# Optimization experiments

Measured on AMD Instinct MI355X. Metric: run time of the kernel, lower is better.

## Reference

```python
import jax, jax.numpy as jnp
import numpy as np

B, SQ, SK, H, A = 4, 512, 512, 256, 128

def setup_inputs() -> dict:
    key = jax.random.key(0)
    ks = jax.random.split(key, 8)
    s = 1.0 / np.sqrt(H)
    sa = 1.0 / np.sqrt(A)
    return {
        "Q": jax.random.normal(ks[0], (B, SQ, H), dtype=jnp.float32),
        "K": jax.random.normal(ks[1], (B, SK, H), dtype=jnp.float32),
        "V": jax.random.normal(ks[2], (B, SK, H), dtype=jnp.float32),
        "W_q": jax.random.uniform(ks[3], (H, A), jnp.float32, -s, s),
        "W_k": jax.random.uniform(ks[4], (H, A), jnp.float32, -s, s),
        "v": jax.random.uniform(ks[5], (A,), jnp.float32, -sa, sa),
        "W_o": jax.random.uniform(ks[6], (H, H), jnp.float32, -s, s),
        "b_o": jax.random.uniform(ks[7], (H,), jnp.float32, -s, s),
    }

def reference(Q, K, V, W_q, W_k, v, W_o, b_o):
    # Q: (B, Sq, H), K/V: (B, Sk, H)
    Qt = Q @ W_q                      # (B, Sq, A)
    Kt = K @ W_k                      # (B, Sk, A)
    additive = jnp.tanh(Qt[:, :, None, :] + Kt[:, None, :, :])  # (B, Sq, Sk, A)
    scores = jnp.einsum('bqka,a->bqk', additive, v)             # (B, Sq, Sk)
    weights = jax.nn.softmax(scores, axis=-1)                   # (B, Sq, Sk)
    out = jnp.einsum('bqk,bkh->bqh', weights, V)                 # (B, Sq, H)
    out = out @ W_o + b_o
    return (out, weights)
```

## Files before the change

### kernel.cpp

```cpp
#include <hip/hip_runtime.h>
#include <math.h>

#define BB 4
#define SQL 512
#define SKL 512
#define HH 256
#define AA 128

#define PRESCALE 2.8853900817779268f

__device__ inline void fma4(float4& a, float s, const float4& b) {
    a.x = fmaf(s, b.x, a.x); a.y = fmaf(s, b.y, a.y);
    a.z = fmaf(s, b.z, a.z); a.w = fmaf(s, b.w, a.w);
}

__device__ inline unsigned short f_to_bf16(float f) {
    unsigned u = __float_as_uint(f);
    return (unsigned short)((u + 0x7fffu + ((u >> 16) & 1u)) >> 16);
}
__device__ inline float4 bf16x4_to_f4(uint2 u) {
    float4 r;
    r.x = __uint_as_float(u.x << 16);
    r.y = __uint_as_float(u.x & 0xffff0000u);
    r.z = __uint_as_float(u.y << 16);
    r.w = __uint_as_float(u.y & 0xffff0000u);
    return r;
}

__global__ __launch_bounds__(256) void prep_kernel(
    const float* __restrict__ Q, const float* __restrict__ K,
    const float* __restrict__ V,
    const float* __restrict__ Wq, const float* __restrict__ Wk,
    const float* __restrict__ Wo,
    float* __restrict__ Qt, float* __restrict__ Kt,
    unsigned short* __restrict__ VW)
{
    __shared__ float rows[16 * 260];
    __shared__ float wbuf[2][32 * 64];
    int tid = threadIdx.x;
    int bid = blockIdx.x;

    const float* X; const float* W;
    int ldW, col0, r0, kind;
    if (bid < 256)      { X=Q; W=Wq; ldW=AA; kind=0; r0=(bid>>1)*16;       col0=(bid&1)*64; }
    else if (bid < 512) { X=K; W=Wk; ldW=AA; kind=1; r0=((bid-256)>>1)*16; col0=((bid-256)&1)*64; }
    else { int b2=bid-512; X=V; W=Wo; ldW=HH; kind=2; r0=(b2>>2)*16;       col0=(b2&3)*64; }

    {
        const float4* Xv = (const float4*)(X + (size_t)r0 * HH);
        #pragma unroll
        for (int it = 0; it < 4; ++it) {
            int l = tid + it * 256;
            int rr = l >> 6, cc = (l & 63) << 2;
            *(float4*)&rows[rr * 260 + cc] = Xv[l];
        }
    }

    float4 wpf0, wpf1;
    {
        int l0 = tid, l1 = tid + 256;
        wpf0 = *(const float4*)(W + (size_t)(l0 >> 4) * ldW + col0 + ((l0 & 15) << 2));
        wpf1 = *(const float4*)(W + (size_t)(l1 >> 4) * ldW + col0 + ((l1 & 15) << 2));
    }

    int r  = tid >> 4;
    int c4 = tid & 15;
    float4 acc = {0.f, 0.f, 0.f, 0.f};

    for (int c = 0; c < 8; ++c) {
        {
            float4* wb = (float4*)&wbuf[c & 1][0];
            wb[tid]       = wpf0;
            wb[tid + 256] = wpf1;
            if (c < 7) {
                const float* Wb = W + (size_t)((c + 1) * 32) * ldW + col0;
                int l0 = tid, l1 = tid + 256;
                wpf0 = *(const float4*)(Wb + (size_t)(l0 >> 4) * ldW + ((l0 & 15) << 2));
                wpf1 = *(const float4*)(Wb + (size_t)(l1 >> 4) * ldW + ((l1 & 15) << 2));
            }
        }
        __syncthreads();
        const float* rrow = &rows[r * 260 + c * 32];
        const float* wb2  = &wbuf[c & 1][c4 << 2];
        #pragma unroll
        for (int h = 0; h < 32; ++h) {
            float rv  = rrow[h];
            float4 w4 = *(const float4*)(wb2 + h * 64);
            fma4(acc, rv, w4);
        }
    }

    if (kind < 2) {
        float* Y = (kind == 0) ? Qt : Kt;
        acc.x *= PRESCALE; acc.y *= PRESCALE; acc.z *= PRESCALE; acc.w *= PRESCALE;
        *(float4*)(Y + (size_t)(r0 + r) * AA + col0 + (c4 << 2)) = acc;
    } else {
        ushort4 s = { f_to_bf16(acc.x), f_to_bf16(acc.y),
                      f_to_bf16(acc.z), f_to_bf16(acc.w) };
        *(ushort4*)(VW + (size_t)(r0 + r) * HH + col0 + (c4 << 2)) = s;
    }
}

__global__ __launch_bounds__(256) void score_part(
    const float* __restrict__ Qt, const float* __restrict__ Kt,
    const float* __restrict__ v,  float* __restrict__ scores)
{
    __shared__ float sc[2][256];

    int tid = threadIdx.x;
    int bid = blockIdx.x;
    int b    = bid >> 9;
    int rem  = bid & 511;
    int q0   = rem & ~1;
    int half = rem & 1;
    int ag = tid & 15;
    int kl = tid >> 4;

    float q0r[8], dr[8], v2[8];
    {
        const float4* vp  = (const float4*)(v + ag * 8);
        const float4* qp0 = (const float4*)(Qt + (size_t)(b * SQL + q0)     * AA + ag * 8);
        const float4* qp1 = (const float4*)(Qt + (size_t)(b * SQL + q0 + 1) * AA + ag * 8);
        #pragma unroll
        for (int j4 = 0; j4 < 2; ++j4) {
            float4 vv4 = vp[j4];
            float4 a0  = qp0[j4];
            float4 a1  = qp1[j4];
            *(float4*)&q0r[j4 * 4] = a0;
            dr[j4*4+0] = __builtin_amdgcn_exp2f(a1.x - a0.x);
            dr[j4*4+1] = __builtin_amdgcn_exp2f(a1.y - a0.y);
            dr[j4*4+2] = __builtin_amdgcn_exp2f(a1.z - a0.z);
            dr[j4*4+3] = __builtin_amdgcn_exp2f(a1.w - a0.w);
            v2[j4*4+0] = 2.0f * vv4.x;
            v2[j4*4+1] = 2.0f * vv4.y;
            v2[j4*4+2] = 2.0f * vv4.z;
            v2[j4*4+3] = 2.0f * vv4.w;
        }
    }

    float S_all;
    {
        float ls = 0.f;
        #pragma unroll
        for (int j = 0; j < 8; ++j) ls += v2[j];
        ls += __shfl_xor(ls, 1);
        ls += __shfl_xor(ls, 2);
        ls += __shfl_xor(ls, 4);
        ls += __shfl_xor(ls, 8);
        S_all = 0.5f * ls;
    }

    const float4* kp = (const float4*)(Kt + (size_t)(b * SKL + half * 256 + kl) * AA + ag * 8);
    float4 n0 = kp[0], n1 = kp[1];
    for (int c = 0; c < 16; ++c) {
        float kt[8];
        *(float4*)&kt[0] = n0;
        *(float4*)&kt[4] = n1;
        if (c < 15) {
            const float4* np = kp + (size_t)(c + 1) * 16 * (AA / 4);
            n0 = np[0]; n1 = np[1];
        }
        float p0 = 0.f, p1 = 0.f;
        #pragma unroll
        for (int j = 0; j < 8; ++j) {
            float x0 = q0r[j] + kt[j];
            float e0 = __builtin_amdgcn_exp2f(x0);
            float e1 = e0 * dr[j];
            float r0 = __builtin_amdgcn_rcpf(e0 + 1.0f);
            float r1 = __builtin_amdgcn_rcpf(e1 + 1.0f);
            p0 = fmaf(v2[j], r0, p0);
            p1 = fmaf(v2[j], r1, p1);
        }
        p0 += __shfl_xor(p0, 1); p1 += __shfl_xor(p1, 1);
        p0 += __shfl_xor(p0, 2); p1 += __shfl_xor(p1, 2);
        p0 += __shfl_xor(p0, 4); p1 += __shfl_xor(p1, 4);
        p0 += __shfl_xor(p0, 8); p1 += __shfl_xor(p1, 8);
        if (ag == 0) {
            sc[0][c * 16 + kl] = S_all - p0;
            sc[1][c * 16 + kl] = S_all - p1;
        }
    }
    __syncthreads();

    if (tid < 128) {
        int q = tid >> 6, i = tid & 63;
        float4 val = *(float4*)&sc[q][i << 2];
        *(float4*)(scores + (size_t)(b * SQL + q0 + q) * SKL + half * 256 + (i << 2)) = val;
    }
}

__global__ __launch_bounds__(256) void softepi_kernel(
    const unsigned short* __restrict__ VW, const float* __restrict__ bo,
    float* __restrict__ weights, float* __restrict__ out)
{
    __shared__ float sw[2][SKL];
    __shared__ float pout[4][2][HH];
    __shared__ float pm[2][2], ps[2][2];

    int tid = threadIdx.x;
    int b  = blockIdx.x >> 8;
    int q0 = (blockIdx.x & 255) << 1;
    int wave = tid >> 6, lane = tid & 63;
    int qi = wave & 1, half = wave >> 1;

    {
        float* wrow = weights + (size_t)(b * SQL + q0 + qi) * SKL + half * 256;
        float4 sv = *(float4*)(wrow + (lane << 2));
        float m = fmaxf(fmaxf(sv.x, sv.y), fmaxf(sv.z, sv.w));
        #pragma unroll
        for (int off = 32; off; off >>= 1) m = fmaxf(m, __shfl_xor(m, off));
        if (lane == 0) pm[qi][half] = m;
        __syncthreads();
        float M = fmaxf(pm[qi][0], pm[qi][1]);
        float4 e;
        e.x = __builtin_amdgcn_exp2f((sv.x - M) * 1.44269504f);
        e.y = __builtin_amdgcn_exp2f((sv.y - M) * 1.44269504f);
        e.z = __builtin_amdgcn_exp2f((sv.z - M) * 1.44269504f);
        e.w = __builtin_amdgcn_exp2f((sv.w - M) * 1.44269504f);
        float s = (e.x + e.y) + (e.z + e.w);
        #pragma unroll
        for (int off = 32; off; off >>= 1) s += __shfl_xor(s, off);
        if (lane == 0) ps[qi][half] = s;
        __syncthreads();
        float rinv = 1.0f / (ps[qi][0] + ps[qi][1]);
        float4 w4 = { e.x * rinv, e.y * rinv, e.z * rinv, e.w * rinv };
        *(float4*)&sw[qi][half * 256 + (lane << 2)] = w4;
        *(float4*)(wrow + (lane << 2)) = w4;
    }
    __syncthreads();

    {
        const uint2* VWb = (const uint2*)(VW + (size_t)b * SKL * HH);
        float4 a0 = {0,0,0,0}, a1 = {0,0,0,0};
        int kbase = wave * 128;
        #pragma unroll 4
        for (int k = 0; k < 128; ++k) {
            int kk = kbase + k;
            uint2 u = VWb[(size_t)kk * (HH / 4) + lane];
            float4 vw4 = bf16x4_to_f4(u);
            float w0 = sw[0][kk];
            float w1 = sw[1][kk];
            fma4(a0, w0, vw4);
            fma4(a1, w1, vw4);
        }
        *(float4*)&pout[wave][0][lane << 2] = a0;
        *(float4*)&pout[wave][1][lane << 2] = a1;
    }
    __syncthreads();
    {
        int h = tid;
        float bias = bo[h];
        #pragma unroll
        for (int q2 = 0; q2 < 2; ++q2) {
            float s = bias + pout[0][q2][h] + pout[1][q2][h]
                           + pout[2][q2][h] + pout[3][q2][h];
            out[(size_t)(b * SQL + q0 + q2) * HH + h] = s;
        }
    }
}

extern "C" void kernel_launch(void* const* d_in, const int* in_sizes, int n_in,
                              void* d_out, int out_size, void* d_ws, size_t ws_size,
                              hipStream_t stream)
{
    const float* Q  = (const float*)d_in[0];
    const float* K  = (const float*)d_in[1];
    const float* V  = (const float*)d_in[2];
    const float* Wq = (const float*)d_in[3];
    const float* Wk = (const float*)d_in[4];
    const float* v  = (const float*)d_in[5];
    const float* Wo = (const float*)d_in[6];
    const float* bo = (const float*)d_in[7];

    float* out     = (float*)d_out;
    float* weights = out + (size_t)BB * SQL * HH;

    float* Qt = (float*)d_ws;
    float* Kt = Qt + (size_t)BB * SQL * AA;
    unsigned short* VW = (unsigned short*)(Kt + (size_t)BB * SKL * AA);

    prep_kernel <<<1024, 256, 0, stream>>>(Q, K, V, Wq, Wk, Wo, Qt, Kt, VW);
    score_part  <<<2048, 256, 0, stream>>>(Qt, Kt, v, weights);
    softepi_kernel<<<1024, 256, 0, stream>>>(VW, bo, weights, out);
}
```

Measured before the change: 130.8 us.

## Register-tile prep GEMM, widen score lanes, vectorize weight reads in epilogue

The projection kernel now keeps W tiles in registers with double-buffered global loads. It stores X transposed in LDS so each thread computes two output rows by 4 columns, and it halves the grid. The score kernel gives each thread 16 attention dimensions instead of 8, which drops one shuffle stage per reduction but raises register use. The softmax-epilogue loop reads weights as float4 and issues four VW loads per iteration for more memory-level parallelism.

```diff
diff --git a/kernel.cpp b/kernel.cpp
--- a/kernel.cpp
+++ b/kernel.cpp
@@ -35,69 +35,92 @@
     float* __restrict__ Qt, float* __restrict__ Kt,
     unsigned short* __restrict__ VW)
 {
-    __shared__ float rows[16 * 260];
-    __shared__ float wbuf[2][32 * 64];
+    __shared__ float rowsT[256 * 18 + 2];
     int tid = threadIdx.x;
     int bid = blockIdx.x;
 
     const float* X; const float* W;
     int ldW, col0, r0, kind;
-    if (bid < 256)      { X=Q; W=Wq; ldW=AA; kind=0; r0=(bid>>1)*16;       col0=(bid&1)*64; }
-    else if (bid < 512) { X=K; W=Wk; ldW=AA; kind=1; r0=((bid-256)>>1)*16; col0=((bid-256)&1)*64; }
-    else { int b2=bid-512; X=V; W=Wo; ldW=HH; kind=2; r0=(b2>>2)*16;       col0=(b2&3)*64; }
+    if (bid < 128)      { X=Q; W=Wq; ldW=AA; kind=0; r0=bid*16;        col0=0; }
+    else if (bid < 256) { X=K; W=Wk; ldW=AA; kind=1; r0=(bid-128)*16;  col0=0; }
+    else { int b2=bid-256; X=V; W=Wo; ldW=HH; kind=2; r0=(b2>>1)*16; col0=(b2&1)*128; }
+
+    int mg = tid >> 5;
+    int n4 = tid & 31;
+    int rpair = mg << 1;
+    const float* Wg = W + col0 + (n4 << 2);
+
+    float4 wA[8], wB[8];
+    #pragma unroll
+    for (int j = 0; j < 8; ++j)
+        wA[j] = *(const float4*)(Wg + (size_t)j * ldW);
 
     {
         const float4* Xv = (const float4*)(X + (size_t)r0 * HH);
         #pragma unroll
         for (int it = 0; it < 4; ++it) {
             int l = tid + it * 256;
-            int rr = l >> 6, cc = (l & 63) << 2;
-            *(float4*)&rows[rr * 260 + cc] = Xv[l];
-        }
-    }
-
-    float4 wpf0, wpf1;
-    {
-        int l0 = tid, l1 = tid + 256;
-        wpf0 = *(const float4*)(W + (size_t)(l0 >> 4) * ldW + col0 + ((l0 & 15) << 2));
-        wpf1 = *(const float4*)(W + (size_t)(l1 >> 4) * ldW + col0 + ((l1 & 15) << 2));
-    }
-
-    int r  = tid >> 4;
-    int c4 = tid & 15;
-    float4 acc = {0.f, 0.f, 0.f, 0.f};
-
-    for (int c = 0; c < 8; ++c) {
+            int r = l >> 6, h4 = (l & 63) << 2;
+            float4 x = Xv[l];
+            rowsT[(h4 + 0) * 18 + r] = x.x;
+            rowsT[(h4 + 1) * 18 + r] = x.y;
+            rowsT[(h4 + 2) * 18 + r] = x.z;
+            rowsT[(h4 + 3) * 18 + r] = x.w;
+        }
+    }
+    __syncthreads();
+
+    float2 aA[8], aB[8];
+    #pragma unroll
+    for (int j = 0; j < 8; ++j)
+        aA[j] = *(const float2*)&rowsT[j * 18 + rpair];
+
+    float4 accA = {0,0,0,0}, accB = {0,0,0,0};
+
+    for (int g = 0; g < 32; g += 2) {
         {
-            float4* wb = (float4*)&wbuf[c & 1][0];
-            wb[tid]       = wpf0;
-            wb[tid + 256] = wpf1;
-            if (c < 7) {
-                const float* Wb = W + (size_t)((c + 1) * 32) * ldW + col0;
-                int l0 = tid, l1 = tid + 256;
-                wpf0 = *(const float4*)(Wb + (size_t)(l0 >> 4) * ldW + ((l0 & 15) << 2));
-                wpf1 = *(const float4*)(Wb + (size_t)(l1 >> 4) * ldW + ((l1 & 15) << 2));
+            const float* Wb = Wg + (size_t)((g + 1) * 8) * ldW;
+            int hb = (g + 1) * 8;
+            #pragma unroll
+            for (int j = 0; j < 8; ++j) {
+                wB[j] = *(const float4*)(Wb + (size_t)j * ldW);
+                aB[j] = *(const float2*)&rowsT[(hb + j) * 18 + rpair];
             }
         }
-        __syncthreads();
-        const float* rrow = &rows[r * 260 + c * 32];
-        const float* wb2  = &wbuf[c & 1][c4 << 2];
-        #pragma unroll
-        for (int h = 0; h < 32; ++h) {
-            float rv  = rrow[h];
-            float4 w4 = *(const float4*)(wb2 + h * 64);
-            fma4(acc, rv, w4);
+        #pragma unroll
+        for (int j = 0; j < 8; ++j) {
+            fma4(accA, aA[j].x, wA[j]);
+            fma4(accB, aA[j].y, wA[j]);
+        }
+        if (g + 2 < 32) {
+            const float* Wb = Wg + (size_t)((g + 2) * 8) * ldW;
+            int hb = (g + 2) * 8;
+            #pragma unroll
+            for (int j = 0; j < 8; ++j) {
+                wA[j] = *(const float4*)(Wb + (size_t)j * ldW);
+                aA[j] = *(const float2*)&rowsT[(hb + j) * 18 + rpair];
+            }
+        }
+        #pragma unroll
+        for (int j = 0; j < 8; ++j) {
+            fma4(accA, aB[j].x, wB[j]);
+            fma4(accB, aB[j].y, wB[j]);
         }
     }
 
     if (kind < 2) {
         float* Y = (kind == 0) ? Qt : Kt;
-        acc.x *= PRESCALE; acc.y *= PRESCALE; acc.z *= PRESCALE; acc.w *= PRESCALE;
-        *(float4*)(Y + (size_t)(r0 + r) * AA + col0 + (c4 << 2)) = acc;
+        accA.x *= PRESCALE; accA.y *= PRESCALE; accA.z *= PRESCALE; accA.w *= PRESCALE;
+        accB.x *= PRESCALE; accB.y *= PRESCALE; accB.z *= PRESCALE; accB.w *= PRESCALE;
+        *(float4*)(Y + (size_t)(r0 + rpair)     * AA + (n4 << 2)) = accA;
+        *(float4*)(Y + (size_t)(r0 + rpair + 1) * AA + (n4 << 2)) = accB;
     } else {
-        ushort4 s = { f_to_bf16(acc.x), f_to_bf16(acc.y),
-                      f_to_bf16(acc.z), f_to_bf16(acc.w) };
-        *(ushort4*)(VW + (size_t)(r0 + r) * HH + col0 + (c4 << 2)) = s;
+        ushort4 sa = { f_to_bf16(accA.x), f_to_bf16(accA.y),
+                       f_to_bf16(accA.z), f_to_bf16(accA.w) };
+        ushort4 sb = { f_to_bf16(accB.x), f_to_bf16(accB.y),
+                       f_to_bf16(accB.z), f_to_bf16(accB.w) };
+        *(ushort4*)(VW + (size_t)(r0 + rpair)     * HH + col0 + (n4 << 2)) = sa;
+        *(ushort4*)(VW + (size_t)(r0 + rpair + 1) * HH + col0 + (n4 << 2)) = sb;
     }
 }
 
@@ -113,16 +136,16 @@
     int rem  = bid & 511;
     int q0   = rem & ~1;
     int half = rem & 1;
-    int ag = tid & 15;
-    int kl = tid >> 4;
-
-    float q0r[8], dr[8], v2[8];
-    {
-        const float4* vp  = (const float4*)(v + ag * 8);
-        const float4* qp0 = (const float4*)(Qt + (size_t)(b * SQL + q0)     * AA + ag * 8);
-        const float4* qp1 = (const float4*)(Qt + (size_t)(b * SQL + q0 + 1) * AA + ag * 8);
-        #pragma unroll
-        for (int j4 = 0; j4 < 2; ++j4) {
+    int ag = tid & 7;
+    int kl = tid >> 3;
+
+    float q0r[16], dr[16], v2[16];
+    {
+        const float4* vp  = (const float4*)(v + ag * 16);
+        const float4* qp0 = (const float4*)(Qt + (size_t)(b * SQL + q0)     * AA + ag * 16);
+        const float4* qp1 = (const float4*)(Qt + (size_t)(b * SQL + q0 + 1) * AA + ag * 16);
+        #pragma unroll
+        for (int j4 = 0; j4 < 4; ++j4) {
             float4 vv4 = vp[j4];
             float4 a0  = qp0[j4];
             float4 a1  = qp1[j4];
@@ -142,27 +165,29 @@
     {
         float ls = 0.f;
         #pragma unroll
-        for (int j = 0; j < 8; ++j) ls += v2[j];
+        for (int j = 0; j < 16; ++j) ls += v2[j];
         ls += __shfl_xor(ls, 1);
         ls += __shfl_xor(ls, 2);
         ls += __shfl_xor(ls, 4);
-        ls += __shfl_xor(ls, 8);
         S_all = 0.5f * ls;
     }
 
-    const float4* kp = (const float4*)(Kt + (size_t)(b * SKL + half * 256 + kl) * AA + ag * 8);
-    float4 n0 = kp[0], n1 = kp[1];
-    for (int c = 0; c < 16; ++c) {
-        float kt[8];
-        *(float4*)&kt[0] = n0;
-        *(float4*)&kt[4] = n1;
-        if (c < 15) {
-            const float4* np = kp + (size_t)(c + 1) * 16 * (AA / 4);
-            n0 = np[0]; n1 = np[1];
-        }
+    const float4* kp = (const float4*)(Kt + (size_t)(b * SKL + half * 256 + kl) * AA + ag * 16);
+    float4 n0 = kp[0], n1 = kp[1], n2 = kp[2], n3 = kp[3];
+    for (int c = 0; c < 8; ++c) {
+        float kt[16];
+        *(float4*)&kt[0]  = n0;
+        *(float4*)&kt[4]  = n1;
+        *(float4*)&kt[8]  = n2;
+        *(float4*)&kt[12] = n3;
+        if (c < 7) {
+            const float4* np = kp + (size_t)(c + 1) * 32 * (AA / 4);
+            n0 = np[0]; n1 = np[1]; n2 = np[2]; n3 = np[3];
+        }
+
         float p0 = 0.f, p1 = 0.f;
         #pragma unroll
-        for (int j = 0; j < 8; ++j) {
+        for (int j = 0; j < 16; ++j) {
             float x0 = q0r[j] + kt[j];
             float e0 = __builtin_amdgcn_exp2f(x0);
             float e1 = e0 * dr[j];
@@ -174,10 +199,9 @@
         p0 += __shfl_xor(p0, 1); p1 += __shfl_xor(p1, 1);
         p0 += __shfl_xor(p0, 2); p1 += __shfl_xor(p1, 2);
         p0 += __shfl_xor(p0, 4); p1 += __shfl_xor(p1, 4);
-        p0 += __shfl_xor(p0, 8); p1 += __shfl_xor(p1, 8);
         if (ag == 0) {
-            sc[0][c * 16 + kl] = S_all - p0;
-            sc[1][c * 16 + kl] = S_all - p1;
+            sc[0][c * 32 + kl] = S_all - p0;
+            sc[1][c * 32 + kl] = S_all - p1;
         }
     }
     __syncthreads();
@@ -233,15 +257,22 @@
         const uint2* VWb = (const uint2*)(VW + (size_t)b * SKL * HH);
         float4 a0 = {0,0,0,0}, a1 = {0,0,0,0};
         int kbase = wave * 128;
-        #pragma unroll 4
-        for (int k = 0; k < 128; ++k) {
-            int kk = kbase + k;
-            uint2 u = VWb[(size_t)kk * (HH / 4) + lane];
-            float4 vw4 = bf16x4_to_f4(u);
-            float w0 = sw[0][kk];
-            float w1 = sw[1][kk];
-            fma4(a0, w0, vw4);
-            fma4(a1, w1, vw4);
+        for (int k4 = 0; k4 < 32; ++k4) {
+            int kk = kbase + k4 * 4;
+            float4 w0 = *(const float4*)&sw[0][kk];
+            float4 w1 = *(const float4*)&sw[1][kk];
+            uint2 u0 = VWb[(size_t)(kk + 0) * (HH / 4) + lane];
+            uint2 u1 = VWb[(size_t)(kk + 1) * (HH / 4) + lane];
+            uint2 u2 = VWb[(size_t)(kk + 2) * (HH / 4) + lane];
+            uint2 u3 = VWb[(size_t)(kk + 3) * (HH / 4) + lane];
+            float4 v0 = bf16x4_to_f4(u0);
+            float4 v1 = bf16x4_to_f4(u1);
+            float4 v2 = bf16x4_to_f4(u2);
+            float4 v3 = bf16x4_to_f4(u3);
+            fma4(a0, w0.x, v0); fma4(a1, w1.x, v0);
+            fma4(a0, w0.y, v1); fma4(a1, w1.y, v1);
+            fma4(a0, w0.z, v2); fma4(a1, w1.z, v2);
+            fma4(a0, w0.w, v3); fma4(a1, w1.w, v3);
         }
         *(float4*)&pout[wave][0][lane << 2] = a0;
         *(float4*)&pout[wave][1][lane << 2] = a1;
@@ -279,7 +310,7 @@
     float* Kt = Qt + (size_t)BB * SQL * AA;
     unsigned short* VW = (unsigned short*)(Kt + (size_t)BB * SKL * AA);
 
-    prep_kernel <<<1024, 256, 0, stream>>>(Q, K, V, Wq, Wk, Wo, Qt, Kt, VW);
-    score_part  <<<2048, 256, 0, stream>>>(Qt, Kt, v, weights);
+    prep_kernel   <<<512, 256, 0, stream>>>(Q, K, V, Wq, Wk, Wo, Qt, Kt, VW);
+    score_part    <<<2048, 256, 0, stream>>>(Qt, Kt, v, weights);
     softepi_kernel<<<1024, 256, 0, stream>>>(VW, bo, weights, out);
 }
```

After: 135.8 us. +3.8%, slower.
